# Performance work log

Measured on AMD Instinct MI355X. Metric: run time of the kernel, lower is better.

Reference implementation:

```python
import jax, jax.numpy as jnp
import numpy as np

MARGIN = 1.0


def setup_inputs() -> dict:
    key = jax.random.key(0)
    k1, k2 = jax.random.split(key)
    B, D = 512, 128
    embeddings = jax.random.normal(k1, (B, D), dtype=jnp.float32)
    labels = jax.random.randint(k2, (B,), 0, 8, dtype=jnp.int64)
    return {"embeddings": embeddings, "labels": labels}


def _triplet_loss(embeddings, labels, margin=MARGIN):
    B = embeddings.shape[0]
    # pairwise euclidean distances (cdist p=2)
    sq = jnp.sum(embeddings * embeddings, axis=1)
    d2 = sq[:, None] + sq[None, :] - 2.0 * (embeddings @ embeddings.T)
    dist = jnp.sqrt(jnp.maximum(d2, 0.0))  # [B, B]

    same = labels[:, None] == labels[None, :]
    eye = jnp.eye(B, dtype=bool)
    pos_mask = same & ~eye          # [B, B] valid positives per anchor
    neg_mask = ~same                # [B, B] valid negatives per anchor
    has_neg = jnp.any(neg_mask, axis=1)  # [B]

    rows = jnp.arange(B)
    # hardest negative per anchor (fallback when no semi-hard negative exists)
    hard_idx = jnp.argmin(jnp.where(neg_mask, dist, jnp.inf), axis=1)  # [B]

    keys = jax.random.split(jax.random.key(42), B)  # one key per positive index p

    def step(carry, xs):
        p, k = xs
        loss_sum, cnt = carry
        pos_d = dist[:, p]                               # [B] anchor->positive dist
        valid = pos_mask[:, p] & has_neg                 # anchor i uses p as positive
        # semi-hard: negative strictly between pos_d and pos_d + margin
        sh = neg_mask & (dist > pos_d[:, None]) & (dist < pos_d[:, None] + margin)
        has_sh = jnp.any(sh, axis=1)
        # uniform random choice among semi-hard negatives via gumbel-argmax
        g = jax.random.gumbel(k, (B, B), dtype=jnp.float32)
        sel = jnp.argmax(jnp.where(sh, g, -jnp.inf), axis=1)
        idx = jnp.where(has_sh, sel, hard_idx)           # [B] chosen negative
        neg_d = dist[rows, idx]
        tl = jax.nn.relu(pos_d - neg_d + margin)
        m = valid & (tl > 0)
        loss_sum = loss_sum + jnp.sum(jnp.where(m, tl, 0.0))
        cnt = cnt + jnp.sum(m.astype(jnp.int32))
        return (loss_sum, cnt), None

    init = (jnp.float32(0.0), jnp.int32(0))
    (loss_sum, cnt), _ = jax.lax.scan(step, init, (rows, keys))
    return jnp.where(cnt == 0, jnp.float32(0.0), loss_sum / cnt.astype(jnp.float32))


def reference(embeddings, labels):
    return _triplet_loss(embeddings, labels)
```

## Files before the change

### kernel.cpp

```cpp
#include <hip/hip_runtime.h>
#include <stdint.h>

#define B 512
#define D 128
#define HALFC 131072u
#define SUB 2
#define NSLOT (SUB * 8)
#define NPART (B * SUB)

__device__ __forceinline__ uint32_t rotl32(uint32_t x, uint32_t r) {
  return (x << r) | (x >> (32u - r));
}

__device__ __forceinline__ void threefry2x32(uint32_t k0, uint32_t k1,
                                             uint32_t x0, uint32_t x1,
                                             uint32_t& y0, uint32_t& y1) {
  uint32_t k2 = k0 ^ k1 ^ 0x1BD11BDAu;
  x0 += k0; x1 += k1;
#define TF_R(r) { x0 += x1; x1 = rotl32(x1, r); x1 ^= x0; }
  TF_R(13) TF_R(15) TF_R(26) TF_R(6)
  x0 += k1; x1 += k2 + 1u;
  TF_R(17) TF_R(29) TF_R(16) TF_R(24)
  x0 += k2; x1 += k0 + 2u;
  TF_R(13) TF_R(15) TF_R(26) TF_R(6)
  x0 += k0; x1 += k1 + 3u;
  TF_R(17) TF_R(29) TF_R(16) TF_R(24)
  x0 += k1; x1 += k2 + 4u;
  TF_R(13) TF_R(15) TF_R(26) TF_R(6)
  x0 += k2; x1 += k0 + 5u;
#undef TF_R
  y0 = x0; y1 = x1;
}

template <int N>
__device__ __forceinline__ void tf_multi(uint32_t k0, uint32_t k1,
                                         uint32_t (&x0)[N], uint32_t (&x1)[N]) {
  uint32_t k2 = k0 ^ k1 ^ 0x1BD11BDAu;
#pragma unroll
  for (int q = 0; q < N; ++q) { x0[q] += k0; x1[q] += k1; }
#define TFM_R(r) \
  _Pragma("unroll") for (int q = 0; q < N; ++q) { \
    x0[q] += x1[q]; x1[q] = rotl32(x1[q], r); x1[q] ^= x0[q]; }
#define TFM_INJ(a, b, c) \
  _Pragma("unroll") for (int q = 0; q < N; ++q) { x0[q] += a; x1[q] += b + c; }
  TFM_R(13) TFM_R(15) TFM_R(26) TFM_R(6)
  TFM_INJ(k1, k2, 1u)
  TFM_R(17) TFM_R(29) TFM_R(16) TFM_R(24)
  TFM_INJ(k2, k0, 2u)
  TFM_R(13) TFM_R(15) TFM_R(26) TFM_R(6)
  TFM_INJ(k0, k1, 3u)
  TFM_R(17) TFM_R(29) TFM_R(16) TFM_R(24)
  TFM_INJ(k1, k2, 4u)
  TFM_R(13) TFM_R(15) TFM_R(26) TFM_R(6)
  TFM_INJ(k2, k0, 5u)
#undef TFM_R
#undef TFM_INJ
}

__device__ __forceinline__ uint32_t dpp_max_all(uint32_t x) {
  uint32_t t;
#define DPP_STEP(ctrl) \
  t = (uint32_t)__builtin_amdgcn_update_dpp(0, (int)x, ctrl, 0xf, 0xf, true); \
  x = (t > x) ? t : x;
  DPP_STEP(0x111)
  DPP_STEP(0x112)
  DPP_STEP(0x114)
  DPP_STEP(0x118)
  DPP_STEP(0x142)
  DPP_STEP(0x143)
#undef DPP_STEP
  return (uint32_t)__builtin_amdgcn_readlane((int)x, 63);
}

__global__ __launch_bounds__(256) void dist_kernel(
    const float* __restrict__ emb, float* __restrict__ dist,
    uint32_t* __restrict__ keys0, uint32_t* __restrict__ keys1) {
  __shared__ float As[32][132];
  __shared__ float Bs[32][132];
  __shared__ float sqa[32], sqb[32];
  int bid = blockIdx.x;
  int ti = bid >> 4, tj = bid & 15;
  int t = threadIdx.x;

  const float4* ga = reinterpret_cast<const float4*>(emb + (size_t)ti * 32 * D);
  const float4* gb = reinterpret_cast<const float4*>(emb + (size_t)tj * 32 * D);
  #pragma unroll
  for (int k = 0; k < 4; ++k) {
    int idx = t + k * 256;
    int r = idx >> 5;
    int c4 = idx & 31;
    *reinterpret_cast<float4*>(&As[r][c4 * 4]) = ga[idx];
    *reinterpret_cast<float4*>(&Bs[r][c4 * 4]) = gb[idx];
  }
  __syncthreads();

  {
    int row = t >> 2, seg = t & 3;
    const float* src = (row < 32) ? &As[row][seg * 32] : &Bs[row - 32][seg * 32];
    float s = 0.f;
    #pragma unroll
    for (int m = 0; m < 32; ++m) { float v = src[m]; s += v * v; }
    s += __shfl_xor(s, 1);
    s += __shfl_xor(s, 2);
    if (seg == 0) { if (row < 32) sqa[row] = s; else sqb[row - 32] = s; }
  }

  int r = t >> 3, g = t & 7;
  const float4* A4 = reinterpret_cast<const float4*>(&As[r][0]);
  const float4* B0 = reinterpret_cast<const float4*>(&Bs[g][0]);
  const float4* B1 = reinterpret_cast<const float4*>(&Bs[g + 8][0]);
  const float4* B2 = reinterpret_cast<const float4*>(&Bs[g + 16][0]);
  const float4* B3 = reinterpret_cast<const float4*>(&Bs[g + 24][0]);
  float acc0 = 0.f, acc1 = 0.f, acc2 = 0.f, acc3 = 0.f;
  #pragma unroll 8
  for (int k4 = 0; k4 < 32; ++k4) {
    float4 a = A4[k4];
    float4 b0 = B0[k4], b1 = B1[k4], b2 = B2[k4], b3 = B3[k4];
    acc0 += a.x * b0.x + a.y * b0.y + a.z * b0.z + a.w * b0.w;
    acc1 += a.x * b1.x + a.y * b1.y + a.z * b1.z + a.w * b1.w;
    acc2 += a.x * b2.x + a.y * b2.y + a.z * b2.z + a.w * b2.w;
    acc3 += a.x * b3.x + a.y * b3.y + a.z * b3.z + a.w * b3.w;
  }
  __syncthreads();
  float sa = sqa[r];
  float* drow = dist + (size_t)(ti * 32 + r) * B + tj * 32;
  drow[g]      = sqrtf(fmaxf(sa + sqb[g]      - 2.f * acc0, 0.f));
  drow[g + 8]  = sqrtf(fmaxf(sa + sqb[g + 8]  - 2.f * acc1, 0.f));
  drow[g + 16] = sqrtf(fmaxf(sa + sqb[g + 16] - 2.f * acc2, 0.f));
  drow[g + 24] = sqrtf(fmaxf(sa + sqb[g + 24] - 2.f * acc3, 0.f));

  if (bid == 0) {
    #pragma unroll
    for (int pp = 0; pp < 2; ++pp) {
      int p = t + pp * 256;
      uint32_t i0 = 2u * (uint32_t)p, i1 = i0 + 1u;
      uint32_t a0, a1, b0, b1;
      if (p < 256) {
        threefry2x32(0u, 42u, i0, i0 + 512u, a0, a1);
        threefry2x32(0u, 42u, i1, i1 + 512u, b0, b1);
        keys0[p] = a0; keys1[p] = b0;
      } else {
        threefry2x32(0u, 42u, i0 - 512u, i0, a0, a1);
        threefry2x32(0u, 42u, i1 - 512u, i1, b0, b1);
        keys0[p] = a1; keys1[p] = b1;
      }
    }
  }
}

__global__ __launch_bounds__(512) void triplet_kernel(
    const float* __restrict__ dist, const int* __restrict__ labels,
    const uint32_t* __restrict__ keys0, const uint32_t* __restrict__ keys1,
    double* __restrict__ partials, int* __restrict__ pcnt) {
  __shared__ float drow[B];
  __shared__ unsigned short slab[B];
  __shared__ uint2 skeys[B];
  __shared__ unsigned short list_sh[B];
  __shared__ uint32_t hist[B];
  __shared__ uint32_t offs[B];
  __shared__ uint32_t cur[B];
  __shared__ unsigned long long skey_arr[B];
  __shared__ uint32_t wsum32[8];
  __shared__ uint32_t wprefix[8];
  __shared__ int nlist_sh;
  __shared__ double lsum[8];
  __shared__ unsigned int lcnt[8];

  int bid = blockIdx.x;
  int i = bid >> 1;
  int sub = bid & 1;
  int t = threadIdx.x;
  slab[t] = (unsigned short)labels[t];
  drow[t] = dist[(size_t)i * B + t];
  skeys[t] = make_uint2(keys0[t], keys1[t]);
  hist[t] = 0u;
  __syncthreads();

  int wave = t >> 6, lane = t & 63;
  unsigned long long lmask_lt = (1ull << lane) - 1ull;
  unsigned short lab_i = slab[i];

  if (wave == 0) {
    int n = 0;
    #pragma unroll
    for (int c = 0; c < 8; ++c) {
      int r = c * 64 + lane;
      bool v = (slab[r] == lab_i);
      unsigned long long mk = __ballot(v);
      if (v) list_sh[n + __popcll(mk & lmask_lt)] = (unsigned short)r;
      n += __popcll(mk);
    }
    if (lane == 0) nlist_sh = (n == B) ? 0 : n;
  }

  float dv_t = drow[t];
  bool neg_t = (slab[t] != lab_i);
  int b_t = (int)fminf(fmaxf(dv_t * 16.0f, 0.0f), 511.0f);
  if (neg_t) atomicAdd(&hist[b_t], 1u);

  unsigned long long hkey = ~0ull;
  #pragma unroll
  for (int jc = 0; jc < 8; ++jc) {
    int j = jc * 64 + lane;
    float dv = drow[j];
    if (slab[j] != lab_i) {
      unsigned long long kk =
          (((unsigned long long)__float_as_uint(dv)) << 9) | (unsigned)j;
      if (kk < hkey) hkey = kk;
    }
  }
  #pragma unroll
  for (int off = 32; off; off >>= 1) {
    unsigned long long o = __shfl_xor(hkey, off);
    if (o < hkey) hkey = o;
  }
  int hard = (int)(hkey & 0x1FFu);
  __syncthreads();

  uint32_t v = hist[t];
  #pragma unroll
  for (int d = 1; d < 64; d <<= 1) {
    uint32_t u = __shfl_up(v, d);
    if (lane >= (unsigned)d) v += u;
  }
  if (lane == 63) wsum32[wave] = v;
  __syncthreads();
  if (t == 0) {
    uint32_t acc = 0;
    #pragma unroll
    for (int w = 0; w < 8; ++w) { wprefix[w] = acc; acc += wsum32[w]; }
  }
  __syncthreads();
  uint32_t inc = v + wprefix[wave];
  offs[t] = inc;
  cur[t] = inc - hist[t];
  __syncthreads();
  if (neg_t) {
    uint32_t pos = atomicAdd(&cur[b_t], 1u);
    skey_arr[pos] =
        (((unsigned long long)__float_as_uint(dv_t)) << 9) | (unsigned)t;
  }
  uint32_t rowbase = (uint32_t)((i & 255) * B);
  bool take_hi = (i >= 256);
  __syncthreads();

  int nlist = nlist_sh;
  double wsum = 0.0;
  unsigned int wcnt = 0;

#define LOAD_ANCHOR(KK, KP, PD) { \
    int p_ = list_sh[KK]; \
    p_ = __builtin_amdgcn_readfirstlane(p_); \
    KP = skeys[p_]; \
    PD = (p_ == i) ? -2.0f : drow[p_];  }

#define DRAIN(NCH) { \
    uint32_t xs0[NCH], xs1[NCH], js[NCH]; bool vd[NCH]; \
    _Pragma("unroll") for (int q = 0; q < NCH; ++q) { \
      int c_ = c0 + q * 64; \
      unsigned long long kv = skey_arr[(c_ < end) ? c_ : start]; \
      vd[q] = (c_ < end) && (kv > lokey) && (kv < hikey); \
      js[q] = (uint32_t)(kv & 0x1FFu); \
      xs0[q] = rowbase + js[q]; \
      xs1[q] = rowbase + js[q] + HALFC; \
    } \
    tf_multi<NCH>(kp.x, kp.y, xs0, xs1); \
    _Pragma("unroll") for (int q = 0; q < NCH; ++q) { \
      uint32_t kk = ((take_hi ? xs1[q] : xs0[q]) & 0xFFFFFE00u) | \
                    (511u - js[q]); \
      if (vd[q] && kk > best) best = kk; \
    } }

  int k = sub * 8 + wave;
  uint2 kpN; float pdN;
  if (k < nlist) LOAD_ANCHOR(k, kpN, pdN);

  while (k < nlist) {
    uint2 kp = kpN;
    float pos_d = pdN;
    int kn = k + NSLOT;
    if (kn < nlist) LOAD_ANCHOR(kn, kpN, pdN);
    float hi_f = pos_d + 1.0f;

    int lo_b = (int)fminf(fmaxf(pos_d * 16.0f, 0.0f), 511.0f);
    int hi_b = (int)fminf(fmaxf(hi_f * 16.0f, 0.0f), 511.0f);
    int start = (int)(offs[lo_b] - hist[lo_b]);
    int end = (int)offs[hi_b];
    unsigned long long lokey =
        (((unsigned long long)__float_as_uint(pos_d)) << 9) | 511u;
    unsigned long long hikey =
        ((unsigned long long)__float_as_uint(hi_f)) << 9;

    float tl;
    if (end > start) {
      uint32_t best = 0u;
      int nch = (end - start + 63) >> 6;
      int c0 = start + lane;
      while (nch > 4) { DRAIN(4); c0 += 256; nch -= 4; }
      switch (nch) {
        case 4: DRAIN(4); break;
        case 3: DRAIN(3); break;
        case 2: DRAIN(2); break;
        default: DRAIN(1); break;
      }
      best = dpp_max_all(best);
      int idx = best ? (511 - (int)(best & 0x1FFu)) : hard;
      tl = pos_d - drow[idx] + 1.0f;
    } else {
      tl = pos_d - drow[hard] + 1.0f;
    }
    if (tl > 0.f) { wsum += (double)tl; wcnt++; }
    k = kn;
  }
#undef LOAD_ANCHOR
#undef DRAIN

  if (lane == 0) { lsum[wave] = wsum; lcnt[wave] = wcnt; }
  __syncthreads();
  if (t == 0) {
    double s = 0.0;
    unsigned int c = 0;
    #pragma unroll
    for (int w = 0; w < 8; ++w) { s += lsum[w]; c += lcnt[w]; }
    partials[bid] = s;
    pcnt[bid] = (int)c;
  }
}

__global__ __launch_bounds__(256) void finalize_kernel(
    const double* __restrict__ partials, const int* __restrict__ pcnt,
    float* __restrict__ out) {
  __shared__ double ss[256];
  __shared__ int sc[256];
  int t = threadIdx.x;
  double s = 0.0;
  int c = 0;
  for (int k = t; k < NPART; k += 256) { s += partials[k]; c += pcnt[k]; }
  ss[t] = s; sc[t] = c;
  __syncthreads();
  for (int st = 128; st; st >>= 1) {
    if (t < st) { ss[t] += ss[t + st]; sc[t] += sc[t + st]; }
    __syncthreads();
  }
  if (t == 0) out[0] = sc[0] ? (float)(ss[0] / (double)sc[0]) : 0.0f;
}

extern "C" void kernel_launch(void* const* d_in, const int* in_sizes, int n_in,
                              void* d_out, int out_size, void* d_ws, size_t ws_size,
                              hipStream_t stream) {
  const float* emb = (const float*)d_in[0];
  const int* labels = (const int*)d_in[1];
  float* out = (float*)d_out;
  char* ws = (char*)d_ws;

  float* dist = (float*)ws;
  uint32_t* keys0 = (uint32_t*)(ws + 1048576);
  uint32_t* keys1 = (uint32_t*)(ws + 1048576 + 2048);
  double* partials = (double*)(ws + 1048576 + 4096);
  int* pcnt = (int*)(ws + 1048576 + 4096 + 8192);

  dist_kernel<<<256, 256, 0, stream>>>(emb, dist, keys0, keys1);
  triplet_kernel<<<B * SUB, 512, 0, stream>>>(dist, labels, keys0, keys1,
                                              partials, pcnt);
  finalize_kernel<<<1, 256, 0, stream>>>(partials, pcnt, out);
}
```

Before: 36.41 us.

## Split per-anchor preprocessing into a separate kernel and spread anchors over waves

Moves the per-row histogram bucketing, sorted negative keys, bucket ranges, hardest-negative distance and per-label positive lists into a new prep kernel that writes them to global memory. The triplet kernel then becomes 256-thread blocks in which each wave independently handles one of sixteen slots of a row, reading the precomputed data from global memory instead of rebuilding it in shared memory. The intent is to avoid recomputing the sort once per sub-block and to remove block-level syncs, so waves can spread across more CUs. In exchange it adds a kernel launch, about 3 MB of global scratch traffic, and global-memory latency in the inner drain loop.

```diff
diff --git a/kernel.cpp b/kernel.cpp
--- a/kernel.cpp
+++ b/kernel.cpp
@@ -4,9 +4,7 @@
 #define B 512
 #define D 128
 #define HALFC 131072u
-#define SUB 2
-#define NSLOT (SUB * 8)
-#define NPART (B * SUB)
+#define NPART 8192
 
 __device__ __forceinline__ uint32_t rotl32(uint32_t x, uint32_t r) {
   return (x << r) | (x >> (32u - r));
@@ -148,75 +146,44 @@
   }
 }
 
-__global__ __launch_bounds__(512) void triplet_kernel(
+__global__ __launch_bounds__(512) void prep_kernel(
     const float* __restrict__ dist, const int* __restrict__ labels,
-    const uint32_t* __restrict__ keys0, const uint32_t* __restrict__ keys1,
-    double* __restrict__ partials, int* __restrict__ pcnt) {
-  __shared__ float drow[B];
+    unsigned long long* __restrict__ skey_g, uint32_t* __restrict__ range_g,
+    float* __restrict__ hard_d_g, unsigned short* __restrict__ lists,
+    int* __restrict__ lcount) {
+  __shared__ uint32_t hist[B];
+  __shared__ uint32_t cur[B];
+  __shared__ uint32_t wsum32[8], wprefix[8];
+  __shared__ unsigned long long wmin[8];
   __shared__ unsigned short slab[B];
-  __shared__ uint2 skeys[B];
-  __shared__ unsigned short list_sh[B];
-  __shared__ uint32_t hist[B];
-  __shared__ uint32_t offs[B];
-  __shared__ uint32_t cur[B];
-  __shared__ unsigned long long skey_arr[B];
-  __shared__ uint32_t wsum32[8];
-  __shared__ uint32_t wprefix[8];
-  __shared__ int nlist_sh;
-  __shared__ double lsum[8];
-  __shared__ unsigned int lcnt[8];
-
-  int bid = blockIdx.x;
-  int i = bid >> 1;
-  int sub = bid & 1;
+  int i = blockIdx.x;
   int t = threadIdx.x;
+  int wave = t >> 6, lane = t & 63;
+  hist[t] = 0u;
   slab[t] = (unsigned short)labels[t];
-  drow[t] = dist[(size_t)i * B + t];
-  skeys[t] = make_uint2(keys0[t], keys1[t]);
-  hist[t] = 0u;
-  __syncthreads();
-
-  int wave = t >> 6, lane = t & 63;
-  unsigned long long lmask_lt = (1ull << lane) - 1ull;
+  float dv = dist[(size_t)i * B + t];
+  __syncthreads();
   unsigned short lab_i = slab[i];
-
-  if (wave == 0) {
-    int n = 0;
-    #pragma unroll
-    for (int c = 0; c < 8; ++c) {
-      int r = c * 64 + lane;
-      bool v = (slab[r] == lab_i);
-      unsigned long long mk = __ballot(v);
-      if (v) list_sh[n + __popcll(mk & lmask_lt)] = (unsigned short)r;
-      n += __popcll(mk);
-    }
-    if (lane == 0) nlist_sh = (n == B) ? 0 : n;
-  }
-
-  float dv_t = drow[t];
-  bool neg_t = (slab[t] != lab_i);
-  int b_t = (int)fminf(fmaxf(dv_t * 16.0f, 0.0f), 511.0f);
-  if (neg_t) atomicAdd(&hist[b_t], 1u);
-
-  unsigned long long hkey = ~0ull;
-  #pragma unroll
-  for (int jc = 0; jc < 8; ++jc) {
-    int j = jc * 64 + lane;
-    float dv = drow[j];
-    if (slab[j] != lab_i) {
-      unsigned long long kk =
-          (((unsigned long long)__float_as_uint(dv)) << 9) | (unsigned)j;
-      if (kk < hkey) hkey = kk;
-    }
-  }
+  bool neg = (slab[t] != lab_i);
+  int b_t = (int)fminf(fmaxf(dv * 16.0f, 0.0f), 511.0f);
+  if (neg) atomicAdd(&hist[b_t], 1u);
+  unsigned long long hkey =
+      neg ? ((((unsigned long long)__float_as_uint(dv)) << 9) | (unsigned)t)
+          : ~0ull;
   #pragma unroll
   for (int off = 32; off; off >>= 1) {
     unsigned long long o = __shfl_xor(hkey, off);
     if (o < hkey) hkey = o;
   }
-  int hard = (int)(hkey & 0x1FFu);
-  __syncthreads();
-
+  if (lane == 0) wmin[wave] = hkey;
+  __syncthreads();
+  if (t == 0) {
+    unsigned long long m = wmin[0];
+    #pragma unroll
+    for (int w = 1; w < 8; ++w)
+      if (wmin[w] < m) m = wmin[w];
+    hard_d_g[i] = __uint_as_float((uint32_t)(m >> 9));
+  }
   uint32_t v = hist[t];
   #pragma unroll
   for (int d = 1; d < 64; d <<= 1) {
@@ -232,64 +199,96 @@
   }
   __syncthreads();
   uint32_t inc = v + wprefix[wave];
-  offs[t] = inc;
-  cur[t] = inc - hist[t];
-  __syncthreads();
-  if (neg_t) {
+  uint32_t st = inc - hist[t];
+  cur[t] = st;
+  range_g[(size_t)i * B + t] = (st << 16) | inc;
+  __syncthreads();
+  if (neg) {
     uint32_t pos = atomicAdd(&cur[b_t], 1u);
-    skey_arr[pos] =
-        (((unsigned long long)__float_as_uint(dv_t)) << 9) | (unsigned)t;
-  }
+    skey_g[(size_t)i * B + pos] =
+        (((unsigned long long)__float_as_uint(dv)) << 9) | (unsigned)t;
+  }
+  if (i == 0) {
+    unsigned long long lmask_lt = (1ull << lane) - 1ull;
+    int n = 0;
+    #pragma unroll
+    for (int c = 0; c < 8; ++c) {
+      int r = c * 64 + lane;
+      bool vv = (slab[r] == (unsigned short)wave);
+      unsigned long long mk = __ballot(vv);
+      if (vv) lists[wave * B + n + __popcll(mk & lmask_lt)] = (unsigned short)r;
+      n += __popcll(mk);
+    }
+    if (lane == 0) lcount[wave] = (n == B) ? 0 : n;
+  }
+}
+
+__global__ __launch_bounds__(256) void triplet_kernel(
+    const float* __restrict__ dist, const int* __restrict__ labels,
+    const uint32_t* __restrict__ keys0, const uint32_t* __restrict__ keys1,
+    const unsigned long long* __restrict__ skey_g,
+    const uint32_t* __restrict__ range_g, const float* __restrict__ hard_d_g,
+    const unsigned short* __restrict__ lists, const int* __restrict__ lcount,
+    double* __restrict__ partials, int* __restrict__ pcnt) {
+  int wave = threadIdx.x >> 6, lane = threadIdx.x & 63;
+  int slot = blockIdx.x * 4 + wave;
+  int i = slot >> 4;
+  int s = slot & 15;
+  int lab = labels[i];
+  int nlist = lcount[lab];
+  const unsigned short* __restrict__ mylist = lists + lab * B;
+  const unsigned long long* __restrict__ skey = skey_g + (size_t)i * B;
+  const uint32_t* __restrict__ range = range_g + (size_t)i * B;
+  const float* __restrict__ drow = dist + (size_t)i * B;
+  float hard_d = hard_d_g[i];
   uint32_t rowbase = (uint32_t)((i & 255) * B);
   bool take_hi = (i >= 256);
-  __syncthreads();
-
-  int nlist = nlist_sh;
   double wsum = 0.0;
   unsigned int wcnt = 0;
 
-#define LOAD_ANCHOR(KK, KP, PD) { \
-    int p_ = list_sh[KK]; \
-    p_ = __builtin_amdgcn_readfirstlane(p_); \
-    KP = skeys[p_]; \
-    PD = (p_ == i) ? -2.0f : drow[p_];  }
+#define LOAD_ANCHOR(KK, KP0, KP1, PD, ST, EN, LOK, HIK) { \
+    int p_ = __builtin_amdgcn_readfirstlane((int)mylist[KK]); \
+    KP0 = keys0[p_]; KP1 = keys1[p_]; \
+    PD = (p_ == i) ? -2.0f : drow[p_];  \
+    float hf_ = PD + 1.0f;  \
+    int lob_ = (int)fminf(fmaxf(PD * 16.0f, 0.0f), 511.0f); \
+    int hib_ = (int)fminf(fmaxf(hf_ * 16.0f, 0.0f), 511.0f); \
+    ST = (int)(range[lob_] >> 16); \
+    EN = (int)(range[hib_] & 0xFFFFu); \
+    LOK = (((unsigned long long)__float_as_uint(PD)) << 9) | 511u; \
+    HIK = ((unsigned long long)__float_as_uint(hf_)) << 9; }
 
 #define DRAIN(NCH) { \
     uint32_t xs0[NCH], xs1[NCH], js[NCH]; bool vd[NCH]; \
     _Pragma("unroll") for (int q = 0; q < NCH; ++q) { \
       int c_ = c0 + q * 64; \
-      unsigned long long kv = skey_arr[(c_ < end) ? c_ : start]; \
+      unsigned long long kv = skey[(c_ < end) ? c_ : start]; \
       vd[q] = (c_ < end) && (kv > lokey) && (kv < hikey); \
       js[q] = (uint32_t)(kv & 0x1FFu); \
       xs0[q] = rowbase + js[q]; \
       xs1[q] = rowbase + js[q] + HALFC; \
     } \
-    tf_multi<NCH>(kp.x, kp.y, xs0, xs1); \
+    tf_multi<NCH>(kp0, kp1, xs0, xs1); \
     _Pragma("unroll") for (int q = 0; q < NCH; ++q) { \
       uint32_t kk = ((take_hi ? xs1[q] : xs0[q]) & 0xFFFFFE00u) | \
                     (511u - js[q]); \
       if (vd[q] && kk > best) best = kk; \
     } }
 
-  int k = sub * 8 + wave;
-  uint2 kpN; float pdN;
-  if (k < nlist) LOAD_ANCHOR(k, kpN, pdN);
+  int k = s;
+  uint32_t kpN0 = 0, kpN1 = 0;
+  float pdN = -2.0f;
+  int stN = 0, enN = 0;
+  unsigned long long lokN = 0, hikN = 0;
+  if (k < nlist) LOAD_ANCHOR(k, kpN0, kpN1, pdN, stN, enN, lokN, hikN);
 
   while (k < nlist) {
-    uint2 kp = kpN;
+    uint32_t kp0 = kpN0, kp1 = kpN1;
     float pos_d = pdN;
-    int kn = k + NSLOT;
-    if (kn < nlist) LOAD_ANCHOR(kn, kpN, pdN);
-    float hi_f = pos_d + 1.0f;
-
-    int lo_b = (int)fminf(fmaxf(pos_d * 16.0f, 0.0f), 511.0f);
-    int hi_b = (int)fminf(fmaxf(hi_f * 16.0f, 0.0f), 511.0f);
-    int start = (int)(offs[lo_b] - hist[lo_b]);
-    int end = (int)offs[hi_b];
-    unsigned long long lokey =
-        (((unsigned long long)__float_as_uint(pos_d)) << 9) | 511u;
-    unsigned long long hikey =
-        ((unsigned long long)__float_as_uint(hi_f)) << 9;
+    int start = stN, end = enN;
+    unsigned long long lokey = lokN, hikey = hikN;
+    int kn = k + 16;
+    if (kn < nlist) LOAD_ANCHOR(kn, kpN0, kpN1, pdN, stN, enN, lokN, hikN);
 
     float tl;
     if (end > start) {
@@ -304,10 +303,14 @@
         default: DRAIN(1); break;
       }
       best = dpp_max_all(best);
-      int idx = best ? (511 - (int)(best & 0x1FFu)) : hard;
-      tl = pos_d - drow[idx] + 1.0f;
+      if (best) {
+        int idx = 511 - (int)(best & 0x1FFu);
+        tl = pos_d - drow[idx] + 1.0f;
+      } else {
+        tl = pos_d - hard_d + 1.0f;
+      }
     } else {
-      tl = pos_d - drow[hard] + 1.0f;
+      tl = pos_d - hard_d + 1.0f;
     }
     if (tl > 0.f) { wsum += (double)tl; wcnt++; }
     k = kn;
@@ -315,15 +318,9 @@
 #undef LOAD_ANCHOR
 #undef DRAIN
 
-  if (lane == 0) { lsum[wave] = wsum; lcnt[wave] = wcnt; }
-  __syncthreads();
-  if (t == 0) {
-    double s = 0.0;
-    unsigned int c = 0;
-    #pragma unroll
-    for (int w = 0; w < 8; ++w) { s += lsum[w]; c += lcnt[w]; }
-    partials[bid] = s;
-    pcnt[bid] = (int)c;
+  if (lane == 0) {
+    partials[slot] = wsum;
+    pcnt[slot] = (int)wcnt;
   }
 }
 
@@ -354,13 +351,21 @@
   char* ws = (char*)d_ws;
 
   float* dist = (float*)ws;
-  uint32_t* keys0 = (uint32_t*)(ws + 1048576);
-  uint32_t* keys1 = (uint32_t*)(ws + 1048576 + 2048);
-  double* partials = (double*)(ws + 1048576 + 4096);
-  int* pcnt = (int*)(ws + 1048576 + 4096 + 8192);
+  unsigned long long* skey_g = (unsigned long long*)(ws + (1u << 20));
+  uint32_t* range_g = (uint32_t*)(ws + 3 * (1u << 20));
+  uint32_t* keys0 = (uint32_t*)(ws + 4 * (1u << 20));
+  uint32_t* keys1 = (uint32_t*)(ws + 4 * (1u << 20) + 2048);
+  unsigned short* lists = (unsigned short*)(ws + 4 * (1u << 20) + 4096);
+  int* lcount = (int*)(ws + 4 * (1u << 20) + 12288);
+  float* hard_d_g = (float*)(ws + 4 * (1u << 20) + 12352);
+  double* partials = (double*)(ws + 4 * (1u << 20) + 16384);
+  int* pcnt = (int*)(ws + 4 * (1u << 20) + 16384 + 65536);
 
   dist_kernel<<<256, 256, 0, stream>>>(emb, dist, keys0, keys1);
-  triplet_kernel<<<B * SUB, 512, 0, stream>>>(dist, labels, keys0, keys1,
-                                              partials, pcnt);
+  prep_kernel<<<B, 512, 0, stream>>>(dist, labels, skey_g, range_g, hard_d_g,
+                                     lists, lcount);
+  triplet_kernel<<<2048, 256, 0, stream>>>(dist, labels, keys0, keys1, skey_g,
+                                           range_g, hard_d_g, lists, lcount,
+                                           partials, pcnt);
   finalize_kernel<<<1, 256, 0, stream>>>(partials, pcnt, out);
 }
```

New measurement: 47.96 us, median of 4. 31.7% more time.
